# Kernel optimization log

Measured on AMD Instinct MI355X. Metric: run time of the kernel, lower is better.

## Reference

```python
import jax, jax.numpy as jnp
import numpy as np

LENGTH = 96
HALF = LENGTH // 2
FACTOR = 0.5
IMG = 512  # spatial size implied by hardcoded clamp to 511


def _crop_dim(d):
    # Faithful translation of PositionEnhancedLoss.crop_dim: returns (top, bottom)
    top = d - HALF
    top_rest = jnp.maximum(-top, 0)
    top = jnp.maximum(top, 0)
    bottom = d + HALF
    bottom_rest = jnp.maximum(bottom - (IMG - 1), 0)
    bottom = jnp.minimum(bottom, IMG - 1)
    top = top - bottom_rest
    bottom = bottom + top_rest
    return top, bottom  # window [top, bottom) of width LENGTH


def setup_inputs() -> dict:
    key = jax.random.key(0)
    kx, ky, kp = jax.random.split(key, 3)
    x = jax.random.normal(kx, (64, 3, 512, 512), dtype=jnp.float32)
    y = jax.random.normal(ky, (64, 3, 512, 512), dtype=jnp.float32)
    position = jax.random.randint(kp, (64, 2), 0, 512, dtype=jnp.int64)
    return {"x": x, "y": y, "position": position}


def reference(x, y, position):
    B, C, H, W = x.shape
    ty, by = _crop_dim(position[:, 0])  # rows (dim 2)
    tx, bx = _crop_dim(position[:, 1])  # cols (dim 3)
    idx = jnp.arange(IMG)
    row_mask = (idx[None, :] >= ty[:, None]) & (idx[None, :] < by[:, None])  # [B, H]
    col_mask = (idx[None, :] >= tx[:, None]) & (idx[None, :] < bx[:, None])  # [B, W]
    # [B, 1, H, W] patch mask, broadcast over channels
    mask = (row_mask[:, None, :, None] & col_mask[:, None, None, :]).astype(x.dtype)
    loss = jnp.abs(x - y)  # L1, reduction='none'
    patch_sum = jnp.sum(loss * mask)
    total_sum = jnp.sum(loss)
    rest_sum = total_sum - patch_sum
    patch_numel = B * C * LENGTH * LENGTH
    rest_numel = B * C * H * W - patch_numel
    patch_loss = patch_sum / patch_numel
    rest_loss = rest_sum / rest_numel
    return rest_loss * (1.0 - FACTOR) + FACTOR * patch_loss
```

## Files before the change

### kernel.cpp

```cpp
#include <hip/hip_runtime.h>


#define IMG    512
#define HALF   48
#define B_DIM  64
#define C_DIM  3
#define NELEM  (64u * 3u * 512u * 512u)
#define NV4    (NELEM / 4u)
#define PER_IMG 786432u

__device__ inline void crop_dim(int d, int& top, int& bot) {
    int t = d - HALF;
    int tr = max(-t, 0);
    t = max(t, 0);
    int b = d + HALF;
    int br = max(b - (IMG - 1), 0);
    b = min(b, IMG - 1);
    top = t - br;
    bot = b + tr;
}

__global__ void pel_setup(const int* __restrict__ pos32, double* acc, int4* wins) {
    __shared__ int is64_s;
    const int t = threadIdx.x;
    if (t == 0) {
        int allzero = 1;
        for (int i = 1; i < 2 * B_DIM; i += 2) allzero &= (pos32[i] == 0);
        is64_s = allzero;
        acc[0] = 0.0;
        acc[1] = 0.0;
    }
    __syncthreads();
    const int is64 = is64_s;
    if (t < B_DIM) {
        int r, c;
        if (is64) {
            const long long* p64 = (const long long*)pos32;
            r = (int)p64[2 * t];
            c = (int)p64[2 * t + 1];
        } else {
            r = pos32[2 * t];
            c = pos32[2 * t + 1];
        }
        int ty, by, tx, bx;
        crop_dim(r, ty, by);
        crop_dim(c, tx, bx);
        wins[t] = make_int4(ty, by, tx, bx);
    }
}

__global__ __launch_bounds__(256) void pel_main(const float4* __restrict__ x,
                                                const float4* __restrict__ y,
                                                const int4* __restrict__ wins,
                                                double* acc) {
    const unsigned stride = gridDim.x * blockDim.x;
    float psum = 0.0f, tsum = 0.0f;
    for (unsigned i = blockIdx.x * blockDim.x + threadIdx.x; i < NV4; i += stride) {
        const unsigned e = i * 4u;
        const unsigned b = e / PER_IMG;
        const int r = (int)((e >> 9) & 511u);
        const int c = (int)(e & 511u);
        const float4 xv = x[i];
        const float4 yv = y[i];
        const float a0 = fabsf(xv.x - yv.x);
        const float a1 = fabsf(xv.y - yv.y);
        const float a2 = fabsf(xv.z - yv.z);
        const float a3 = fabsf(xv.w - yv.w);
        tsum += (a0 + a1) + (a2 + a3);
        const int4 w = wins[b];
        if (r >= w.x && r < w.y) {
            float p = 0.0f;
            if (c     >= w.z && c     < w.w) p += a0;
            if (c + 1 >= w.z && c + 1 < w.w) p += a1;
            if (c + 2 >= w.z && c + 2 < w.w) p += a2;
            if (c + 3 >= w.z && c + 3 < w.w) p += a3;
            psum += p;
        }
    }
    #pragma unroll
    for (int off = 32; off > 0; off >>= 1) {
        psum += __shfl_down(psum, off);
        tsum += __shfl_down(tsum, off);
    }
    __shared__ float sp[4], st[4];
    const int wave = threadIdx.x >> 6;
    const int lane = threadIdx.x & 63;
    if (lane == 0) { sp[wave] = psum; st[wave] = tsum; }
    __syncthreads();
    if (threadIdx.x == 0) {
        const float P = (sp[0] + sp[1]) + (sp[2] + sp[3]);
        const float T = (st[0] + st[1]) + (st[2] + st[3]);
        atomicAdd(&acc[0], (double)P);
        atomicAdd(&acc[1], (double)T);
    }
}

__global__ void pel_final(const double* __restrict__ acc, float* __restrict__ out) {
    const double patch_sum = acc[0];
    const double total_sum = acc[1];
    const double rest_sum = total_sum - patch_sum;
    const double patch_numel = (double)B_DIM * C_DIM * 96.0 * 96.0;
    const double total_numel = (double)NELEM;
    const double rest_numel = total_numel - patch_numel;
    const double res = (rest_sum / rest_numel) * 0.5 + 0.5 * (patch_sum / patch_numel);
    out[0] = (float)res;
}

extern "C" void kernel_launch(void* const* d_in, const int* in_sizes, int n_in,
                              void* d_out, int out_size, void* d_ws, size_t ws_size,
                              hipStream_t stream) {
    const float* x = (const float*)d_in[0];
    const float* y = (const float*)d_in[1];
    const int*   pos = (const int*)d_in[2];
    double* acc = (double*)d_ws;
    int4*   wins = (int4*)((char*)d_ws + 16);

    pel_setup<<<1, 64, 0, stream>>>(pos, acc, wins);
    pel_main<<<2048, 256, 0, stream>>>((const float4*)x, (const float4*)y, wins, acc);
    pel_final<<<1, 1, 0, stream>>>(acc, (float*)d_out);
}
```

Before: 425.1 us.

## Unroll grid-stride loads by eight, cache windows in LDS, replace atomics with partials

The main loop now has a compile-time trip count and is unrolled by eight, with all x/y float4 loads issued before any compute so more memory requests are in flight per thread. Crop windows are staged in shared memory, and the range checks use unsigned-compare tricks. The double atomics are replaced by per-block float2 partials that a 256-thread final kernel reduces. This raises register pressure and hardcodes the grid size and trip count to the exact problem size.

```diff
diff --git a/kernel.cpp b/kernel.cpp
--- a/kernel.cpp
+++ b/kernel.cpp
@@ -1,13 +1,18 @@
 #include <hip/hip_runtime.h>
 
 
-#define IMG    512
-#define HALF   48
-#define B_DIM  64
-#define C_DIM  3
-#define NELEM  (64u * 3u * 512u * 512u)
-#define NV4    (NELEM / 4u)
-#define PER_IMG 786432u
+#define IMG     512
+#define HALF    48
+#define B_DIM   64
+#define NELEM   (64u * 3u * 512u * 512u)
+#define NV4     (NELEM / 4u)
+#define THREADS 256
+#define BLOCKS  2048
+#define STRIDE  (BLOCKS * THREADS)
+#define ITERS   (NV4 / STRIDE)
+#define UNROLL  8
+#define OUTER   (ITERS / UNROLL)
+#define IMG_V4  196608u
 
 __device__ inline void crop_dim(int d, int& top, int& bot) {
     int t = d - HALF;
@@ -20,21 +25,18 @@
     bot = b + tr;
 }
 
-__global__ void pel_setup(const int* __restrict__ pos32, double* acc, int4* wins) {
+__global__ void pel_setup(const int* __restrict__ pos32, int4* wins) {
     __shared__ int is64_s;
     const int t = threadIdx.x;
     if (t == 0) {
         int allzero = 1;
         for (int i = 1; i < 2 * B_DIM; i += 2) allzero &= (pos32[i] == 0);
         is64_s = allzero;
-        acc[0] = 0.0;
-        acc[1] = 0.0;
     }
     __syncthreads();
-    const int is64 = is64_s;
     if (t < B_DIM) {
         int r, c;
-        if (is64) {
+        if (is64_s) {
             const long long* p64 = (const long long*)pos32;
             r = (int)p64[2 * t];
             c = (int)p64[2 * t + 1];
@@ -49,34 +51,49 @@
     }
 }
 
-__global__ __launch_bounds__(256) void pel_main(const float4* __restrict__ x,
-                                                const float4* __restrict__ y,
-                                                const int4* __restrict__ wins,
-                                                double* acc) {
-    const unsigned stride = gridDim.x * blockDim.x;
+__global__ __launch_bounds__(THREADS) void pel_main(const float4* __restrict__ x,
+                                                    const float4* __restrict__ y,
+                                                    const int4* __restrict__ wins,
+                                                    float2* __restrict__ partials) {
+    __shared__ int4 s_wins[B_DIM];
+    if (threadIdx.x < B_DIM) s_wins[threadIdx.x] = wins[threadIdx.x];
+    __syncthreads();
+
+    const unsigned base = blockIdx.x * THREADS + threadIdx.x;
     float psum = 0.0f, tsum = 0.0f;
-    for (unsigned i = blockIdx.x * blockDim.x + threadIdx.x; i < NV4; i += stride) {
-        const unsigned e = i * 4u;
-        const unsigned b = e / PER_IMG;
-        const int r = (int)((e >> 9) & 511u);
-        const int c = (int)(e & 511u);
-        const float4 xv = x[i];
-        const float4 yv = y[i];
-        const float a0 = fabsf(xv.x - yv.x);
-        const float a1 = fabsf(xv.y - yv.y);
-        const float a2 = fabsf(xv.z - yv.z);
-        const float a3 = fabsf(xv.w - yv.w);
-        tsum += (a0 + a1) + (a2 + a3);
-        const int4 w = wins[b];
-        if (r >= w.x && r < w.y) {
-            float p = 0.0f;
-            if (c     >= w.z && c     < w.w) p += a0;
-            if (c + 1 >= w.z && c + 1 < w.w) p += a1;
-            if (c + 2 >= w.z && c + 2 < w.w) p += a2;
-            if (c + 3 >= w.z && c + 3 < w.w) p += a3;
-            psum += p;
+
+    #pragma unroll 1
+    for (int o = 0; o < OUTER; ++o) {
+        float4 xv[UNROLL], yv[UNROLL];
+        #pragma unroll
+        for (int u = 0; u < UNROLL; ++u) {
+            const unsigned i = base + (unsigned)(o * UNROLL + u) * STRIDE;
+            xv[u] = x[i];
+            yv[u] = y[i];
+        }
+        #pragma unroll
+        for (int u = 0; u < UNROLL; ++u) {
+            const unsigned i = base + (unsigned)(o * UNROLL + u) * STRIDE;
+            const float a0 = fabsf(xv[u].x - yv[u].x);
+            const float a1 = fabsf(xv[u].y - yv[u].y);
+            const float a2 = fabsf(xv[u].z - yv[u].z);
+            const float a3 = fabsf(xv[u].w - yv[u].w);
+            tsum += (a0 + a1) + (a2 + a3);
+            const unsigned b = i / IMG_V4;
+            const int r = (int)((i >> 7) & 511u);
+            const int c = (int)((i & 127u) << 2);
+            const int4 w = s_wins[b];
+            if ((unsigned)(r - w.x) < 96u) {
+                float p = 0.0f;
+                p += ((unsigned)(c     - w.z) < 96u) ? a0 : 0.0f;
+                p += ((unsigned)(c + 1 - w.z) < 96u) ? a1 : 0.0f;
+                p += ((unsigned)(c + 2 - w.z) < 96u) ? a2 : 0.0f;
+                p += ((unsigned)(c + 3 - w.z) < 96u) ? a3 : 0.0f;
+                psum += p;
+            }
         }
     }
+
     #pragma unroll
     for (int off = 32; off > 0; off >>= 1) {
         psum += __shfl_down(psum, off);
@@ -84,26 +101,39 @@
     }
     __shared__ float sp[4], st[4];
     const int wave = threadIdx.x >> 6;
-    const int lane = threadIdx.x & 63;
-    if (lane == 0) { sp[wave] = psum; st[wave] = tsum; }
+    if ((threadIdx.x & 63) == 0) { sp[wave] = psum; st[wave] = tsum; }
     __syncthreads();
     if (threadIdx.x == 0) {
-        const float P = (sp[0] + sp[1]) + (sp[2] + sp[3]);
-        const float T = (st[0] + st[1]) + (st[2] + st[3]);
-        atomicAdd(&acc[0], (double)P);
-        atomicAdd(&acc[1], (double)T);
+        partials[blockIdx.x] = make_float2((sp[0] + sp[1]) + (sp[2] + sp[3]),
+                                           (st[0] + st[1]) + (st[2] + st[3]));
     }
 }
 
-__global__ void pel_final(const double* __restrict__ acc, float* __restrict__ out) {
-    const double patch_sum = acc[0];
-    const double total_sum = acc[1];
-    const double rest_sum = total_sum - patch_sum;
-    const double patch_numel = (double)B_DIM * C_DIM * 96.0 * 96.0;
-    const double total_numel = (double)NELEM;
-    const double rest_numel = total_numel - patch_numel;
-    const double res = (rest_sum / rest_numel) * 0.5 + 0.5 * (patch_sum / patch_numel);
-    out[0] = (float)res;
+__global__ __launch_bounds__(256) void pel_final(const float2* __restrict__ partials,
+                                                 float* __restrict__ out) {
+    double psum = 0.0, tsum = 0.0;
+    for (int i = threadIdx.x; i < BLOCKS; i += 256) {
+        const float2 v = partials[i];
+        psum += (double)v.x;
+        tsum += (double)v.y;
+    }
+    #pragma unroll
+    for (int off = 32; off > 0; off >>= 1) {
+        psum += __shfl_down(psum, off);
+        tsum += __shfl_down(tsum, off);
+    }
+    __shared__ double sp[4], st[4];
+    const int wave = threadIdx.x >> 6;
+    if ((threadIdx.x & 63) == 0) { sp[wave] = psum; st[wave] = tsum; }
+    __syncthreads();
+    if (threadIdx.x == 0) {
+        const double patch_sum = (sp[0] + sp[1]) + (sp[2] + sp[3]);
+        const double total_sum = (st[0] + st[1]) + (st[2] + st[3]);
+        const double rest_sum = total_sum - patch_sum;
+        const double patch_numel = 64.0 * 3.0 * 96.0 * 96.0;
+        const double rest_numel = (double)NELEM - patch_numel;
+        out[0] = (float)((rest_sum / rest_numel) * 0.5 + 0.5 * (patch_sum / patch_numel));
+    }
 }
 
 extern "C" void kernel_launch(void* const* d_in, const int* in_sizes, int n_in,
@@ -112,10 +142,10 @@
     const float* x = (const float*)d_in[0];
     const float* y = (const float*)d_in[1];
     const int*   pos = (const int*)d_in[2];
-    double* acc = (double*)d_ws;
-    int4*   wins = (int4*)((char*)d_ws + 16);
+    int4*   wins     = (int4*)d_ws;
+    float2* partials = (float2*)((char*)d_ws + 1024);
 
-    pel_setup<<<1, 64, 0, stream>>>(pos, acc, wins);
-    pel_main<<<2048, 256, 0, stream>>>((const float4*)x, (const float4*)y, wins, acc);
-    pel_final<<<1, 1, 0, stream>>>(acc, (float*)d_out);
+    pel_setup<<<1, 64, 0, stream>>>(pos, wins);
+    pel_main<<<BLOCKS, THREADS, 0, stream>>>((const float4*)x, (const float4*)y, wins, partials);
+    pel_final<<<1, 256, 0, stream>>>(partials, (float*)d_out);
 }
```

Result: faster. 403.1 us (-5.2%).
